# Kernel tuning notes

Measured on AMD Instinct MI355X. Metric: run time of the kernel, lower is better.

The kernel has to match this reference:

```python
import jax, jax.numpy as jnp
import numpy as np

RADIUS = 1.3
N_SAMPLES = 256
STEP = 0.0176


def trilinear(grid, pts):
    """grid: [C, D, H, W]; pts: [M, 3] in [-1, 1] ordered (x, y, z) like torch grid_sample
    (x indexes W, y indexes H, z indexes D), align_corners=True, border padding.
    Returns [M, C]."""
    C, D, H, W = grid.shape
    sizes = jnp.asarray([W, H, D], dtype=pts.dtype)
    co = jnp.clip((pts + 1.0) * 0.5 * (sizes - 1.0), 0.0, sizes - 1.0)
    c0 = jnp.floor(co)
    f = co - c0                                   # [M,3] trilinear weights
    i0 = c0.astype(jnp.int32)
    i1 = jnp.minimum(i0 + 1, jnp.asarray([W - 1, H - 1, D - 1], jnp.int32))
    gf = grid.reshape(C, -1)

    def gat(ix, iy, iz):                          # -> [M, C]
        return gf[:, (iz * H + iy) * W + ix].T

    x0, y0, z0 = i0[:, 0], i0[:, 1], i0[:, 2]
    x1, y1, z1 = i1[:, 0], i1[:, 1], i1[:, 2]
    wx, wy, wz = f[:, 0:1], f[:, 1:2], f[:, 2:3]
    out = (gat(x0, y0, z0) * (1 - wx) * (1 - wy) * (1 - wz)
         + gat(x1, y0, z0) * wx       * (1 - wy) * (1 - wz)
         + gat(x0, y1, z0) * (1 - wx) * wy       * (1 - wz)
         + gat(x1, y1, z0) * wx       * wy       * (1 - wz)
         + gat(x0, y0, z1) * (1 - wx) * (1 - wy) * wz
         + gat(x1, y0, z1) * wx       * (1 - wy) * wz
         + gat(x0, y1, z1) * (1 - wx) * wy       * wz
         + gat(x1, y1, z1) * wx       * wy       * wz)
    return out


def get_intersections(rays_o, dirn):
    """Ray / cube[-R,R]^3 intersection; N_SAMPLES uniform steps from entry point.
    Returns pts [B,N,3], t-values [B,N], validity mask [B,N]."""
    eps = 1e-9
    safe_d = jnp.where(jnp.abs(dirn) < eps, eps, dirn)
    inv = 1.0 / safe_d
    t1 = (-RADIUS - rays_o) * inv
    t2 = (RADIUS - rays_o) * inv
    tmin = jnp.max(jnp.minimum(t1, t2), axis=-1)
    tmax = jnp.min(jnp.maximum(t1, t2), axis=-1)
    tnear = jnp.maximum(tmin, 0.0)
    hit = tmax > tnear                                          # [B]
    t = tnear[:, None] + STEP * jnp.arange(N_SAMPLES, dtype=rays_o.dtype)[None, :]
    pts = rays_o[:, None, :] + t[..., None] * dirn[:, None, :]  # [B,N,3]
    mask = (t < tmax[:, None]) & hit[:, None]
    return pts, t, mask


def setup_inputs() -> dict:
    key = jax.random.key(0)
    ks = jax.random.split(key, 12)
    B, R, GD, FD, NF, HW = 2048, 128, 3, 32, 32, 64
    o = jax.random.normal(ks[0], (B, 3), dtype=jnp.float32)
    rays_o = o / jnp.linalg.norm(o, axis=-1, keepdims=True) * (2.0 * RADIUS)
    rays_d = -rays_o + 0.3 * jax.random.normal(ks[1], (B, 3), dtype=jnp.float32)
    G1 = 0.01 * jax.random.normal(ks[2], (GD, R, R, R), dtype=jnp.float32)
    F = 0.05 * jax.random.normal(ks[3], (FD, NF, NF, NF), dtype=jnp.float32)
    s = 0.1
    return {
        'rays_o': rays_o, 'rays_d': rays_d, 'G1': G1, 'F': F,
        'Wd1': s * jax.random.normal(ks[4], (FD, HW), dtype=jnp.float32),
        'bd1': jnp.zeros((HW,), jnp.float32),
        'Wd2': s * jax.random.normal(ks[5], (HW, 1), dtype=jnp.float32),
        'bd2': jnp.zeros((1,), jnp.float32),
        'Wc1': s * jax.random.normal(ks[6], (FD + 3, HW), dtype=jnp.float32),
        'bc1': jnp.zeros((HW,), jnp.float32),
        'Wc2': s * jax.random.normal(ks[7], (HW, 3), dtype=jnp.float32),
        'bc2': jnp.zeros((3,), jnp.float32),
    }


def reference(rays_o, rays_d, G1, F, Wd1, bd1, Wd2, bd2, Wc1, bc1, Wc2, bc2):
    B = rays_o.shape[0]
    dirn = rays_d / jnp.linalg.norm(rays_d, axis=-1, keepdims=True)
    pts, t, mask = get_intersections(rays_o, dirn)           # [B,N,3],[B,N],[B,N]
    pts_n = (pts / RADIUS).reshape(-1, 3)                     # [M,3] in ~[-1,1]

    # nested multi-grid trilinear lookups: coords -> G1 -> F
    g1v = trilinear(G1, pts_n)                                # [M,3]
    feats = trilinear(F, g1v)                                 # [M,feature_dim]

    # density MLP (1 hidden layer, width 64)
    h = jax.nn.relu(feats @ Wd1 + bd1)
    sigma = (h @ Wd2 + bd2)[:, 0].reshape(B, N_SAMPLES)
    sigma = jnp.where(mask, sigma, 0.0)

    # sigma -> alpha -> compositing weights (abs_light)
    dists = jnp.concatenate([t[:, 1:] - t[:, :-1],
                             jnp.full((B, 1), STEP, t.dtype)], axis=1)
    alpha = 1.0 - jnp.exp(-jax.nn.relu(sigma) * dists)
    T = jnp.cumprod(1.0 - alpha + 1e-10, axis=1)
    T_excl = jnp.concatenate([jnp.ones((B, 1), alpha.dtype), T[:, :-1]], axis=1)
    weights = alpha * T_excl                                  # [B,N]

    # color MLP conditioned on view direction
    dflat = jnp.broadcast_to(dirn[:, None, :], (B, N_SAMPLES, 3)).reshape(-1, 3)
    hc = jax.nn.relu(jnp.concatenate([feats, dflat], axis=-1) @ Wc1 + bc1)
    rgb = jax.nn.sigmoid((hc @ Wc2 + bc2).reshape(B, N_SAMPLES, 3))
    rgb = jnp.where(mask[..., None], rgb, 0.0)

    out = jnp.sum(weights[..., None] * rgb, axis=1)           # [B,3]
    acc = jnp.sum(weights, axis=1)
    return out + (1.0 - acc)[:, None]                         # white background
```

## Files before the change

### kernel.cpp

```cpp
#include <hip/hip_runtime.h>
#include <hip/hip_fp16.h>
#include <math.h>

#define NSAMP 256

typedef _Float16 f16;
typedef _Float16 f16x8 __attribute__((ext_vector_type(8)));
typedef float    f32x4 __attribute__((ext_vector_type(4)));

__global__ __launch_bounds__(256) void transpose_F(
    const float* __restrict__ Fg, float* __restrict__ Ft)
{
    const int j = blockIdx.x * 256 + threadIdx.x;
    float4 o[8];
    #pragma unroll
    for (int q = 0; q < 8; ++q) {
        o[q].x = Fg[(size_t)(4*q+0)*32768 + j];
        o[q].y = Fg[(size_t)(4*q+1)*32768 + j];
        o[q].z = Fg[(size_t)(4*q+2)*32768 + j];
        o[q].w = Fg[(size_t)(4*q+3)*32768 + j];
    }
    float4* dst = (float4*)(Ft + (size_t)j * 32);
    #pragma unroll
    for (int q = 0; q < 8; ++q) dst[q] = o[q];
}

__global__ __launch_bounds__(256) void pack_bfrags(
    const float* __restrict__ Wd1, const float* __restrict__ Wc1,
    f16* __restrict__ Bd, f16* __restrict__ Bc)
{
    const int idx  = threadIdx.x;
    const int nt   = idx >> 6;
    const int lane = idx & 63;
    const int j    = nt*16 + (lane & 15);
    const int k0   = (lane >> 4) * 8;
    f16x8 vd, vc;
    #pragma unroll
    for (int i = 0; i < 8; ++i) {
        vd[i] = (f16)Wd1[(k0+i)*64 + j];
        vc[i] = (f16)Wc1[(k0+i)*64 + j];
    }
    *(f16x8*)(Bd + ((size_t)(nt*64+lane))*8) = vd;
    *(f16x8*)(Bc + ((size_t)(nt*64+lane))*8) = vc;
}

template<bool USE_MFMA>
__global__ __launch_bounds__(256) __attribute__((amdgpu_waves_per_eu(2, 6)))
void nerf_fused(
    const float* __restrict__ rays_o, const float* __restrict__ rays_d,
    const float* __restrict__ G1, const float* __restrict__ Fg,
    const float* __restrict__ Wd1, const float* __restrict__ bd1,
    const float* __restrict__ Wd2, const float* __restrict__ bd2,
    const float* __restrict__ Wc1, const float* __restrict__ bc1,
    const float* __restrict__ Wc2, const float* __restrict__ bc2,
    const float* __restrict__ Ft,
    const f16* __restrict__ Bd, const f16* __restrict__ Bc,
    float* __restrict__ out)
{
    const float RADIUS = 1.3f;
    const float STEP = 0.0176f;

    const int b    = blockIdx.x;
    const int tid  = threadIdx.x;
    const int lane = tid & 63;
    const int wv   = tid >> 6;

    __shared__ __align__(16) f16 feats_lds[256][32];
    __shared__ float sig_lds[256];
    __shared__ f16   rgb_lds[256][4];
    __shared__ float s_wtot[4];
    __shared__ float s_red[4][4];

    const float ox = rays_o[b*3+0], oy = rays_o[b*3+1], oz = rays_o[b*3+2];
    const float rdx = rays_d[b*3+0], rdy = rays_d[b*3+1], rdz = rays_d[b*3+2];
    const float rn  = sqrtf(rdx*rdx + rdy*rdy + rdz*rdz);
    const float dxn = rdx/rn, dyn = rdy/rn, dzn = rdz/rn;

    float sd, inv, t1, t2, tmin, tmax;
    sd = (fabsf(dxn) < 1e-9f) ? 1e-9f : dxn; inv = 1.0f/sd;
    t1 = (-RADIUS - ox)*inv; t2 = (RADIUS - ox)*inv;
    tmin = fminf(t1,t2); tmax = fmaxf(t1,t2);
    sd = (fabsf(dyn) < 1e-9f) ? 1e-9f : dyn; inv = 1.0f/sd;
    t1 = (-RADIUS - oy)*inv; t2 = (RADIUS - oy)*inv;
    tmin = fmaxf(tmin, fminf(t1,t2)); tmax = fminf(tmax, fmaxf(t1,t2));
    sd = (fabsf(dzn) < 1e-9f) ? 1e-9f : dzn; inv = 1.0f/sd;
    t1 = (-RADIUS - oz)*inv; t2 = (RADIUS - oz)*inv;
    tmin = fmaxf(tmin, fminf(t1,t2)); tmax = fminf(tmax, fmaxf(t1,t2));

    const float tnear = fmaxf(tmin, 0.0f);
    const bool  hit   = tmax > tnear;
    const float t     = tnear + STEP * (float)tid;
    const bool  mask  = (t < tmax) && hit;

    const bool wave_active = __any(mask);

    float sigma = 0.0f, rr = 0.0f, rg = 0.0f, rb = 0.0f;

    float feats[32];
    if (wave_active) {
        const float invR = 1.0f / RADIUS;
        const float px = (ox + t*dxn) * invR;
        const float py = (oy + t*dyn) * invR;
        const float pz = (oz + t*dzn) * invR;

        float cox = fminf(fmaxf((px+1.0f)*0.5f*127.0f, 0.0f), 127.0f);
        float coy = fminf(fmaxf((py+1.0f)*0.5f*127.0f, 0.0f), 127.0f);
        float coz = fminf(fmaxf((pz+1.0f)*0.5f*127.0f, 0.0f), 127.0f);
        int x0 = (int)floorf(cox); float fx = cox - (float)x0; int x1 = min(x0+1, 127);
        int y0 = (int)floorf(coy); float fy = coy - (float)y0; int y1 = min(y0+1, 127);
        int z0 = (int)floorf(coz); float fz = coz - (float)z0; int z1 = min(z0+1, 127);

        {
            const float wx0 = 1.0f-fx, wx1 = fx;
            const float wy0 = 1.0f-fy, wy1 = fy;
            const float wz0 = 1.0f-fz, wz1 = fz;
            const float w000 = wx0*wy0*wz0, w100 = wx1*wy0*wz0;
            const float w010 = wx0*wy1*wz0, w110 = wx1*wy1*wz0;
            const float w001 = wx0*wy0*wz1, w101 = wx1*wy0*wz1;
            const float w011 = wx0*wy1*wz1, w111 = wx1*wy1*wz1;
            const int i000 = (z0*128 + y0)*128 + x0;
            const int dxo = x1 - x0;
            const int dyo = (y1 - y0)*128;
            const int dzo = (z1 - z0)*16384;
            const int i100 = i000 + dxo,       i010 = i000 + dyo;
            const int i110 = i000 + dyo + dxo, i001 = i000 + dzo;
            const int i101 = i000 + dzo + dxo, i011 = i000 + dzo + dyo;
            const int i111 = i000 + dzo + dyo + dxo;

            float g[3];
            #pragma unroll
            for (int c = 0; c < 3; ++c) {
                const float* gp = G1 + (size_t)c * 2097152;
                g[c] = w000*gp[i000] + w100*gp[i100] + w010*gp[i010] + w110*gp[i110]
                     + w001*gp[i001] + w101*gp[i101] + w011*gp[i011] + w111*gp[i111];
            }

            cox = fminf(fmaxf((g[0]+1.0f)*0.5f*31.0f, 0.0f), 31.0f);
            coy = fminf(fmaxf((g[1]+1.0f)*0.5f*31.0f, 0.0f), 31.0f);
            coz = fminf(fmaxf((g[2]+1.0f)*0.5f*31.0f, 0.0f), 31.0f);
            x0 = (int)floorf(cox); fx = cox - (float)x0; x1 = min(x0+1, 31);
            y0 = (int)floorf(coy); fy = coy - (float)y0; y1 = min(y0+1, 31);
            z0 = (int)floorf(coz); fz = coz - (float)z0; z1 = min(z0+1, 31);
        }

        #pragma unroll
        for (int c = 0; c < 32; ++c) feats[c] = 0.0f;
        {
            const float wx0 = 1.0f-fx, wx1 = fx;
            const float wy0 = 1.0f-fy, wy1 = fy;
            const float wz0 = 1.0f-fz, wz1 = fz;
            const int j000 = (z0*32 + y0)*32 + x0;
            const int dxo = x1 - x0;
            const int dyo = (y1 - y0)*32;
            const int dzo = (z1 - z0)*1024;

            const int   jidx[8] = { j000,           j000+dxo,
                                    j000+dyo,       j000+dyo+dxo,
                                    j000+dzo,       j000+dzo+dxo,
                                    j000+dzo+dyo,   j000+dzo+dyo+dxo };
            const float jwt[8]  = { wx0*wy0*wz0, wx1*wy0*wz0,
                                    wx0*wy1*wz0, wx1*wy1*wz0,
                                    wx0*wy0*wz1, wx1*wy0*wz1,
                                    wx0*wy1*wz1, wx1*wy1*wz1 };

            if (USE_MFMA) {
                #pragma unroll
                for (int corner = 0; corner < 8; ++corner) {
                    const float4* fp = (const float4*)(Ft + (size_t)jidx[corner] * 32);
                    const float w = jwt[corner];
                    #pragma unroll
                    for (int q = 0; q < 8; ++q) {
                        const float4 v = fp[q];
                        feats[4*q+0] += w * v.x;
                        feats[4*q+1] += w * v.y;
                        feats[4*q+2] += w * v.z;
                        feats[4*q+3] += w * v.w;
                    }
                }
            } else {
                #pragma unroll
                for (int corner = 0; corner < 8; ++corner) {
                    const float w = jwt[corner];
                    const int  j  = jidx[corner];
                    #pragma unroll
                    for (int c = 0; c < 32; ++c)
                        feats[c] += w * Fg[(size_t)c * 32768 + j];
                }
            }
        }
    }

    if (USE_MFMA) {
        if (wave_active) {
            #pragma unroll
            for (int gq = 0; gq < 4; ++gq) {
                f16x8 h;
                #pragma unroll
                for (int i = 0; i < 8; ++i) h[i] = (f16)feats[gq*8+i];
                *(f16x8*)&feats_lds[tid][gq*8] = h;
            }
        }
        __syncthreads();

        if (wave_active) {
            const int lane15 = lane & 15;
            const int laneg  = lane >> 4;

            float bias_d[4], bias_c[4], wd2v[4];
            float wc2r[4], wc2g[4], wc2b[4];
            #pragma unroll
            for (int nt = 0; nt < 4; ++nt) {
                const int j = nt*16 + lane15;
                bias_d[nt] = bd1[j];
                bias_c[nt] = bc1[j] + dxn*Wc1[32*64+j] + dyn*Wc1[33*64+j] + dzn*Wc1[34*64+j];
                wd2v[nt]   = Wd2[j];
                wc2r[nt]   = Wc2[j*3+0];
                wc2g[nt]   = Wc2[j*3+1];
                wc2b[nt]   = Wc2[j*3+2];
            }
            f16x8 bdf[4], bcf[4];
            #pragma unroll
            for (int nt = 0; nt < 4; ++nt) {
                bdf[nt] = *(const f16x8*)(Bd + ((size_t)(nt*64+lane))*8);
                bcf[nt] = *(const f16x8*)(Bc + ((size_t)(nt*64+lane))*8);
            }

            #pragma unroll
            for (int mt = 0; mt < 4; ++mt) {
                const int arow = wv*64 + mt*16 + lane15;
                const f16x8 af = *(const f16x8*)&feats_lds[arow][laneg*8];

                f32x4 accd[4], accc[4];
                #pragma unroll
                for (int nt = 0; nt < 4; ++nt) {
                    const float bdv = bias_d[nt], bcv = bias_c[nt];
                    accd[nt] = (f32x4){bdv, bdv, bdv, bdv};
                    accc[nt] = (f32x4){bcv, bcv, bcv, bcv};
                }
                #pragma unroll
                for (int nt = 0; nt < 4; ++nt) {
                    accd[nt] = __builtin_amdgcn_mfma_f32_16x16x32_f16(af, bdf[nt], accd[nt], 0, 0, 0);
                    accc[nt] = __builtin_amdgcn_mfma_f32_16x16x32_f16(af, bcf[nt], accc[nt], 0, 0, 0);
                }

                float ss[4] = {0.f,0.f,0.f,0.f};
                float sr[4] = {0.f,0.f,0.f,0.f};
                float sg[4] = {0.f,0.f,0.f,0.f};
                float sb[4] = {0.f,0.f,0.f,0.f};
                #pragma unroll
                for (int nt = 0; nt < 4; ++nt) {
                    #pragma unroll
                    for (int reg = 0; reg < 4; ++reg) {
                        const float hd = fmaxf(accd[nt][reg], 0.0f);
                        ss[reg] += hd * wd2v[nt];
                        const float hc = fmaxf(accc[nt][reg], 0.0f);
                        sr[reg] += hc * wc2r[nt];
                        sg[reg] += hc * wc2g[nt];
                        sb[reg] += hc * wc2b[nt];
                    }
                }
                #pragma unroll
                for (int st = 1; st < 16; st <<= 1) {
                    #pragma unroll
                    for (int reg = 0; reg < 4; ++reg) {
                        ss[reg] += __shfl_xor(ss[reg], st, 64);
                        sr[reg] += __shfl_xor(sr[reg], st, 64);
                        sg[reg] += __shfl_xor(sg[reg], st, 64);
                        sb[reg] += __shfl_xor(sb[reg], st, 64);
                    }
                }
                if (lane15 == 0) {
                    const int base = wv*64 + mt*16 + laneg*4;
                    #pragma unroll
                    for (int reg = 0; reg < 4; ++reg) {
                        sig_lds[base+reg]    = ss[reg];
                        rgb_lds[base+reg][0] = (f16)sr[reg];
                        rgb_lds[base+reg][1] = (f16)sg[reg];
                        rgb_lds[base+reg][2] = (f16)sb[reg];
                    }
                }
            }
        }
        __syncthreads();

        {
            const float sv  = sig_lds[tid];
            const float crv = (float)rgb_lds[tid][0] + bc2[0];
            const float cgv = (float)rgb_lds[tid][1] + bc2[1];
            const float cbv = (float)rgb_lds[tid][2] + bc2[2];
            sigma = mask ? (sv + bd2[0]) : 0.0f;
            rr = mask ? 1.0f/(1.0f + expf(-crv)) : 0.0f;
            rg = mask ? 1.0f/(1.0f + expf(-cgv)) : 0.0f;
            rb = mask ? 1.0f/(1.0f + expf(-cbv)) : 0.0f;
        }
    } else {
        if (wave_active) {
            float sg1 = bd2[0], cr = 0.0f, cg = 0.0f, cb = 0.0f;
            for (int j0 = 0; j0 < 64; j0 += 8) {
                float ad[8], ac[8];
                #pragma unroll
                for (int jj = 0; jj < 8; ++jj) {
                    ad[jj] = bd1[j0+jj];
                    ac[jj] = bc1[j0+jj] + dxn*Wc1[32*64 + j0 + jj]
                                        + dyn*Wc1[33*64 + j0 + jj]
                                        + dzn*Wc1[34*64 + j0 + jj];
                }
                #pragma unroll
                for (int k = 0; k < 32; ++k) {
                    const float fv = feats[k];
                    #pragma unroll
                    for (int jj = 0; jj < 8; ++jj) {
                        ad[jj] += fv * Wd1[k*64 + j0 + jj];
                        ac[jj] += fv * Wc1[k*64 + j0 + jj];
                    }
                }
                #pragma unroll
                for (int jj = 0; jj < 8; ++jj) {
                    sg1 += fmaxf(ad[jj], 0.0f) * Wd2[j0+jj];
                    const float hc = fmaxf(ac[jj], 0.0f);
                    cr += hc * Wc2[(j0+jj)*3 + 0];
                    cg += hc * Wc2[(j0+jj)*3 + 1];
                    cb += hc * Wc2[(j0+jj)*3 + 2];
                }
            }
            cr += bc2[0]; cg += bc2[1]; cb += bc2[2];
            sigma = mask ? sg1 : 0.0f;
            rr = mask ? 1.0f/(1.0f + expf(-cr)) : 0.0f;
            rg = mask ? 1.0f/(1.0f + expf(-cg)) : 0.0f;
            rb = mask ? 1.0f/(1.0f + expf(-cb)) : 0.0f;
        }
    }

    const float alpha = 1.0f - expf(-fmaxf(sigma, 0.0f) * STEP);
    float p = 1.0f - alpha + 1e-10f;

    float scan = p;
    #pragma unroll
    for (int off = 1; off < 64; off <<= 1) {
        const float n = __shfl_up(scan, off, 64);
        if (lane >= off) scan *= n;
    }
    if (lane == 63) s_wtot[wv] = scan;
    __syncthreads();

    float pre = 1.0f;
    #pragma unroll
    for (int q = 0; q < 4; ++q) if (q < wv) pre *= s_wtot[q];
    float excl = __shfl_up(scan, 1, 64);
    if (lane == 0) excl = 1.0f;
    const float Texcl = pre * excl;

    const float w = alpha * Texcl;
    float sw  = w;
    float swr = w * rr, swg = w * rg, swb = w * rb;

    #pragma unroll
    for (int off = 32; off > 0; off >>= 1) {
        sw  += __shfl_down(sw,  off, 64);
        swr += __shfl_down(swr, off, 64);
        swg += __shfl_down(swg, off, 64);
        swb += __shfl_down(swb, off, 64);
    }
    if (lane == 0) {
        s_red[wv][0] = sw;  s_red[wv][1] = swr;
        s_red[wv][2] = swg; s_red[wv][3] = swb;
    }
    __syncthreads();
    if (tid == 0) {
        float W = 0.0f, R = 0.0f, Gc = 0.0f, Bc2_ = 0.0f;
        #pragma unroll
        for (int q = 0; q < 4; ++q) {
            W  += s_red[q][0]; R  += s_red[q][1];
            Gc += s_red[q][2]; Bc2_ += s_red[q][3];
        }
        const float bg = 1.0f - W;
        out[b*3+0] = R  + bg;
        out[b*3+1] = Gc + bg;
        out[b*3+2] = Bc2_ + bg;
    }
}

extern "C" void kernel_launch(void* const* d_in, const int* in_sizes, int n_in,
                              void* d_out, int out_size, void* d_ws, size_t ws_size,
                              hipStream_t stream) {
    const float* rays_o = (const float*)d_in[0];
    const float* rays_d = (const float*)d_in[1];
    const float* G1     = (const float*)d_in[2];
    const float* Fg     = (const float*)d_in[3];
    const float* Wd1    = (const float*)d_in[4];
    const float* bd1    = (const float*)d_in[5];
    const float* Wd2    = (const float*)d_in[6];
    const float* bd2    = (const float*)d_in[7];
    const float* Wc1    = (const float*)d_in[8];
    const float* bc1    = (const float*)d_in[9];
    const float* Wc2    = (const float*)d_in[10];
    const float* bc2    = (const float*)d_in[11];
    float* out = (float*)d_out;

    const int B = in_sizes[0] / 3;
    const size_t ft_bytes = (size_t)32768 * 32 * sizeof(float);
    const size_t bf_bytes = (size_t)4 * 64 * 8 * sizeof(f16);

    if (ws_size >= ft_bytes + 2*bf_bytes) {
        float* Ft = (float*)d_ws;
        f16*   Bd = (f16*)((char*)d_ws + ft_bytes);
        f16*   Bc = (f16*)((char*)d_ws + ft_bytes + bf_bytes);
        transpose_F<<<dim3(128), dim3(256), 0, stream>>>(Fg, Ft);
        pack_bfrags<<<dim3(1), dim3(256), 0, stream>>>(Wd1, Wc1, Bd, Bc);
        nerf_fused<true><<<dim3(B), dim3(NSAMP), 0, stream>>>(
            rays_o, rays_d, G1, Fg, Wd1, bd1, Wd2, bd2, Wc1, bc1, Wc2, bc2,
            Ft, Bd, Bc, out);
    } else {
        nerf_fused<false><<<dim3(B), dim3(NSAMP), 0, stream>>>(
            rays_o, rays_d, G1, Fg, Wd1, bd1, Wd2, bd2, Wc1, bc1, Wc2, bc2,
            Fg, (const f16*)d_ws, (const f16*)d_ws, out);
    }
}
```

Before: 144.9 us.

## Split fused NeRF kernel into gather+MLP and compositing passes with fp16 interleaved coarse grid

Adds a pre-pass that converts the coarse 3-channel grid G1 into an interleaved fp16x4 layout, so each trilinear corner becomes a single 8-byte load. The fused kernel is split in two. A gather kernel runs the grid lookups and MFMA MLPs, with each wave taking samples from a different ray and whole-wave early exit for missed rays. A second kernel does sigmoid, transmittance scan and compositing. This aims to cut gather traffic and improve load balance and latency hiding. The cost is an extra transpose pass over the 8M-element grid each call, a round-trip of per-sample results through global memory, fp16 rounding of coarse grid values, and a larger workspace requirement.

```diff
diff --git a/kernel.cpp b/kernel.cpp
--- a/kernel.cpp
+++ b/kernel.cpp
@@ -5,6 +5,7 @@
 #define NSAMP 256
 
 typedef _Float16 f16;
+typedef _Float16 f16x4 __attribute__((ext_vector_type(4)));
 typedef _Float16 f16x8 __attribute__((ext_vector_type(8)));
 typedef float    f32x4 __attribute__((ext_vector_type(4)));
 
@@ -23,6 +24,18 @@
     float4* dst = (float4*)(Ft + (size_t)j * 32);
     #pragma unroll
     for (int q = 0; q < 8; ++q) dst[q] = o[q];
+}
+
+__global__ __launch_bounds__(256) void transpose_G1h(
+    const float* __restrict__ G1, f16x4* __restrict__ G1t)
+{
+    const int v = blockIdx.x * 256 + threadIdx.x;
+    f16x4 o;
+    o[0] = (f16)G1[v];
+    o[1] = (f16)G1[2097152 + v];
+    o[2] = (f16)G1[2*2097152 + v];
+    o[3] = (f16)0.0f;
+    G1t[v] = o;
 }
 
 __global__ __launch_bounds__(256) void pack_bfrags(
@@ -42,6 +55,305 @@
     }
     *(f16x8*)(Bd + ((size_t)(nt*64+lane))*8) = vd;
     *(f16x8*)(Bc + ((size_t)(nt*64+lane))*8) = vc;
+}
+
+__global__ __launch_bounds__(256) __attribute__((amdgpu_waves_per_eu(2, 6)))
+void nerf_gather(
+    const float* __restrict__ rays_o, const float* __restrict__ rays_d,
+    const f16x4* __restrict__ G1t, const float* __restrict__ Ft,
+    const float* __restrict__ bd1, const float* __restrict__ Wd2,
+    const float* __restrict__ bd2,
+    const float* __restrict__ Wc1, const float* __restrict__ bc1,
+    const float* __restrict__ Wc2,
+    const f16* __restrict__ Bd, const f16* __restrict__ Bc,
+    float4* __restrict__ samp)
+{
+    const float RADIUS = 1.3f;
+    const float STEP = 0.0176f;
+
+    const int tid  = threadIdx.x;
+    const int lane = tid & 63;
+    const int wv   = tid >> 6;
+
+    int ray = blockIdx.x + wv * (gridDim.x >> 2);
+    if (ray >= (int)gridDim.x) ray -= gridDim.x;
+
+    __shared__ __align__(16) f16 feats_lds[256][40];
+
+    const float ox = rays_o[ray*3+0], oy = rays_o[ray*3+1], oz = rays_o[ray*3+2];
+    const float rdx = rays_d[ray*3+0], rdy = rays_d[ray*3+1], rdz = rays_d[ray*3+2];
+    const float rn  = sqrtf(rdx*rdx + rdy*rdy + rdz*rdz);
+    const float dxn = rdx/rn, dyn = rdy/rn, dzn = rdz/rn;
+
+    float sd, inv, t1, t2, tmin, tmax;
+    sd = (fabsf(dxn) < 1e-9f) ? 1e-9f : dxn; inv = 1.0f/sd;
+    t1 = (-RADIUS - ox)*inv; t2 = (RADIUS - ox)*inv;
+    tmin = fminf(t1,t2); tmax = fmaxf(t1,t2);
+    sd = (fabsf(dyn) < 1e-9f) ? 1e-9f : dyn; inv = 1.0f/sd;
+    t1 = (-RADIUS - oy)*inv; t2 = (RADIUS - oy)*inv;
+    tmin = fmaxf(tmin, fminf(t1,t2)); tmax = fminf(tmax, fmaxf(t1,t2));
+    sd = (fabsf(dzn) < 1e-9f) ? 1e-9f : dzn; inv = 1.0f/sd;
+    t1 = (-RADIUS - oz)*inv; t2 = (RADIUS - oz)*inv;
+    tmin = fmaxf(tmin, fminf(t1,t2)); tmax = fminf(tmax, fmaxf(t1,t2));
+
+    const float tnear = fmaxf(tmin, 0.0f);
+    const bool  hit   = tmax > tnear;
+    const float t     = tnear + STEP * (float)tid;
+    const bool  mask  = (t < tmax) && hit;
+
+    if (!__any(mask)) {
+        samp[(size_t)ray*NSAMP + tid] = (float4){0.f, 0.f, 0.f, 0.f};
+        return;
+    }
+
+    float feats[32];
+    {
+        const float invR = 1.0f / RADIUS;
+        const float px = (ox + t*dxn) * invR;
+        const float py = (oy + t*dyn) * invR;
+        const float pz = (oz + t*dzn) * invR;
+
+        float cox = fminf(fmaxf((px+1.0f)*0.5f*127.0f, 0.0f), 127.0f);
+        float coy = fminf(fmaxf((py+1.0f)*0.5f*127.0f, 0.0f), 127.0f);
+        float coz = fminf(fmaxf((pz+1.0f)*0.5f*127.0f, 0.0f), 127.0f);
+        int x0 = (int)floorf(cox); float fx = cox - (float)x0; int x1 = min(x0+1, 127);
+        int y0 = (int)floorf(coy); float fy = coy - (float)y0; int y1 = min(y0+1, 127);
+        int z0 = (int)floorf(coz); float fz = coz - (float)z0; int z1 = min(z0+1, 127);
+
+        {
+            const float wx0 = 1.0f-fx, wx1 = fx;
+            const float wy0 = 1.0f-fy, wy1 = fy;
+            const float wz0 = 1.0f-fz, wz1 = fz;
+            const float w000 = wx0*wy0*wz0, w100 = wx1*wy0*wz0;
+            const float w010 = wx0*wy1*wz0, w110 = wx1*wy1*wz0;
+            const float w001 = wx0*wy0*wz1, w101 = wx1*wy0*wz1;
+            const float w011 = wx0*wy1*wz1, w111 = wx1*wy1*wz1;
+            const int i000 = (z0*128 + y0)*128 + x0;
+            const int dxo = x1 - x0;
+            const int dyo = (y1 - y0)*128;
+            const int dzo = (z1 - z0)*16384;
+
+            const f16x4 v000 = G1t[i000];
+            const f16x4 v100 = G1t[i000 + dxo];
+            const f16x4 v010 = G1t[i000 + dyo];
+            const f16x4 v110 = G1t[i000 + dyo + dxo];
+            const f16x4 v001 = G1t[i000 + dzo];
+            const f16x4 v101 = G1t[i000 + dzo + dxo];
+            const f16x4 v011 = G1t[i000 + dzo + dyo];
+            const f16x4 v111 = G1t[i000 + dzo + dyo + dxo];
+
+            float g[3];
+            #pragma unroll
+            for (int c = 0; c < 3; ++c) {
+                g[c] = w000*(float)v000[c] + w100*(float)v100[c]
+                     + w010*(float)v010[c] + w110*(float)v110[c]
+                     + w001*(float)v001[c] + w101*(float)v101[c]
+                     + w011*(float)v011[c] + w111*(float)v111[c];
+            }
+
+            cox = fminf(fmaxf((g[0]+1.0f)*0.5f*31.0f, 0.0f), 31.0f);
+            coy = fminf(fmaxf((g[1]+1.0f)*0.5f*31.0f, 0.0f), 31.0f);
+            coz = fminf(fmaxf((g[2]+1.0f)*0.5f*31.0f, 0.0f), 31.0f);
+            x0 = (int)floorf(cox); fx = cox - (float)x0; x1 = min(x0+1, 31);
+            y0 = (int)floorf(coy); fy = coy - (float)y0; y1 = min(y0+1, 31);
+            z0 = (int)floorf(coz); fz = coz - (float)z0; z1 = min(z0+1, 31);
+        }
+
+        #pragma unroll
+        for (int c = 0; c < 32; ++c) feats[c] = 0.0f;
+        {
+            const float wx0 = 1.0f-fx, wx1 = fx;
+            const float wy0 = 1.0f-fy, wy1 = fy;
+            const float wz0 = 1.0f-fz, wz1 = fz;
+            const int j000 = (z0*32 + y0)*32 + x0;
+            const int dxo = x1 - x0;
+            const int dyo = (y1 - y0)*32;
+            const int dzo = (z1 - z0)*1024;
+
+            const int   jidx[8] = { j000,           j000+dxo,
+                                    j000+dyo,       j000+dyo+dxo,
+                                    j000+dzo,       j000+dzo+dxo,
+                                    j000+dzo+dyo,   j000+dzo+dyo+dxo };
+            const float jwt[8]  = { wx0*wy0*wz0, wx1*wy0*wz0,
+                                    wx0*wy1*wz0, wx1*wy1*wz0,
+                                    wx0*wy0*wz1, wx1*wy0*wz1,
+                                    wx0*wy1*wz1, wx1*wy1*wz1 };
+
+            #pragma unroll
+            for (int corner = 0; corner < 8; ++corner) {
+                const float4* fp = (const float4*)(Ft + (size_t)jidx[corner] * 32);
+                const float w = jwt[corner];
+                #pragma unroll
+                for (int q = 0; q < 8; ++q) {
+                    const float4 v = fp[q];
+                    feats[4*q+0] += w * v.x;
+                    feats[4*q+1] += w * v.y;
+                    feats[4*q+2] += w * v.z;
+                    feats[4*q+3] += w * v.w;
+                }
+            }
+        }
+    }
+
+    #pragma unroll
+    for (int gq = 0; gq < 4; ++gq) {
+        f16x8 h;
+        #pragma unroll
+        for (int i = 0; i < 8; ++i) h[i] = (f16)feats[gq*8+i];
+        *(f16x8*)&feats_lds[tid][gq*8] = h;
+    }
+
+    {
+        const int lane15 = lane & 15;
+        const int laneg  = lane >> 4;
+
+        float bias_d[4], bias_c[4], wd2v[4];
+        float wc2r[4], wc2g[4], wc2b[4];
+        #pragma unroll
+        for (int nt = 0; nt < 4; ++nt) {
+            const int j = nt*16 + lane15;
+            bias_d[nt] = bd1[j];
+            bias_c[nt] = bc1[j] + dxn*Wc1[32*64+j] + dyn*Wc1[33*64+j] + dzn*Wc1[34*64+j];
+            wd2v[nt]   = Wd2[j];
+            wc2r[nt]   = Wc2[j*3+0];
+            wc2g[nt]   = Wc2[j*3+1];
+            wc2b[nt]   = Wc2[j*3+2];
+        }
+        f16x8 bdf[4], bcf[4];
+        #pragma unroll
+        for (int nt = 0; nt < 4; ++nt) {
+            bdf[nt] = *(const f16x8*)(Bd + ((size_t)(nt*64+lane))*8);
+            bcf[nt] = *(const f16x8*)(Bc + ((size_t)(nt*64+lane))*8);
+        }
+        const float bd2v = bd2[0];
+
+        #pragma unroll
+        for (int mt = 0; mt < 4; ++mt) {
+            const int arow = wv*64 + mt*16 + lane15;
+            const f16x8 af = *(const f16x8*)&feats_lds[arow][laneg*8];
+
+            f32x4 accd[4], accc[4];
+            #pragma unroll
+            for (int nt = 0; nt < 4; ++nt) {
+                const float bdv = bias_d[nt], bcv = bias_c[nt];
+                accd[nt] = (f32x4){bdv, bdv, bdv, bdv};
+                accc[nt] = (f32x4){bcv, bcv, bcv, bcv};
+            }
+            #pragma unroll
+            for (int nt = 0; nt < 4; ++nt) {
+                accd[nt] = __builtin_amdgcn_mfma_f32_16x16x32_f16(af, bdf[nt], accd[nt], 0, 0, 0);
+                accc[nt] = __builtin_amdgcn_mfma_f32_16x16x32_f16(af, bcf[nt], accc[nt], 0, 0, 0);
+            }
+
+            float ss[4] = {0.f,0.f,0.f,0.f};
+            float sr[4] = {0.f,0.f,0.f,0.f};
+            float sg[4] = {0.f,0.f,0.f,0.f};
+            float sb[4] = {0.f,0.f,0.f,0.f};
+            #pragma unroll
+            for (int nt = 0; nt < 4; ++nt) {
+                #pragma unroll
+                for (int reg = 0; reg < 4; ++reg) {
+                    const float hd = fmaxf(accd[nt][reg], 0.0f);
+                    ss[reg] += hd * wd2v[nt];
+                    const float hc = fmaxf(accc[nt][reg], 0.0f);
+                    sr[reg] += hc * wc2r[nt];
+                    sg[reg] += hc * wc2g[nt];
+                    sb[reg] += hc * wc2b[nt];
+                }
+            }
+            #pragma unroll
+            for (int st = 1; st < 16; st <<= 1) {
+                #pragma unroll
+                for (int reg = 0; reg < 4; ++reg) {
+                    ss[reg] += __shfl_xor(ss[reg], st, 64);
+                    sr[reg] += __shfl_xor(sr[reg], st, 64);
+                    sg[reg] += __shfl_xor(sg[reg], st, 64);
+                    sb[reg] += __shfl_xor(sb[reg], st, 64);
+                }
+            }
+            if (lane15 == 0) {
+                const int base = wv*64 + mt*16 + laneg*4;
+                #pragma unroll
+                for (int reg = 0; reg < 4; ++reg) {
+                    const int   row = base + reg;
+                    const float tr  = tnear + STEP * (float)row;
+                    const bool  mr  = (tr < tmax) && hit;
+                    float4 o;
+                    o.x = mr ? (ss[reg] + bd2v) : 0.0f;
+                    o.y = sr[reg]; o.z = sg[reg]; o.w = sb[reg];
+                    samp[(size_t)ray*NSAMP + row] = o;
+                }
+            }
+        }
+    }
+}
+
+__global__ __launch_bounds__(256) void nerf_comp(
+    const float4* __restrict__ samp, const float* __restrict__ bc2,
+    float* __restrict__ out)
+{
+    const float STEP = 0.0176f;
+    const int b    = blockIdx.x;
+    const int tid  = threadIdx.x;
+    const int lane = tid & 63;
+    const int wv   = tid >> 6;
+
+    __shared__ float s_wtot[4];
+    __shared__ float s_red[4][4];
+
+    const float4 v = samp[(size_t)b*NSAMP + tid];
+    const float sigma = v.x;
+    const float rr = 1.0f/(1.0f + expf(-(v.y + bc2[0])));
+    const float rg = 1.0f/(1.0f + expf(-(v.z + bc2[1])));
+    const float rb = 1.0f/(1.0f + expf(-(v.w + bc2[2])));
+
+    const float alpha = 1.0f - expf(-fmaxf(sigma, 0.0f) * STEP);
+    float p = 1.0f - alpha + 1e-10f;
+
+    float scan = p;
+    #pragma unroll
+    for (int off = 1; off < 64; off <<= 1) {
+        const float n = __shfl_up(scan, off, 64);
+        if (lane >= off) scan *= n;
+    }
+    if (lane == 63) s_wtot[wv] = scan;
+    __syncthreads();
+
+    float pre = 1.0f;
+    #pragma unroll
+    for (int q = 0; q < 4; ++q) if (q < wv) pre *= s_wtot[q];
+    float excl = __shfl_up(scan, 1, 64);
+    if (lane == 0) excl = 1.0f;
+    const float Texcl = pre * excl;
+
+    const float w = alpha * Texcl;
+    float sw  = w;
+    float swr = w * rr, swg = w * rg, swb = w * rb;
+
+    #pragma unroll
+    for (int off = 32; off > 0; off >>= 1) {
+        sw  += __shfl_down(sw,  off, 64);
+        swr += __shfl_down(swr, off, 64);
+        swg += __shfl_down(swg, off, 64);
+        swb += __shfl_down(swb, off, 64);
+    }
+    if (lane == 0) {
+        s_red[wv][0] = sw;  s_red[wv][1] = swr;
+        s_red[wv][2] = swg; s_red[wv][3] = swb;
+    }
+    __syncthreads();
+    if (tid == 0) {
+        float W = 0.0f, R = 0.0f, Gc = 0.0f, Bc_ = 0.0f;
+        #pragma unroll
+        for (int q = 0; q < 4; ++q) {
+            W  += s_red[q][0]; R  += s_red[q][1];
+            Gc += s_red[q][2]; Bc_ += s_red[q][3];
+        }
+        const float bg = 1.0f - W;
+        out[b*3+0] = R   + bg;
+        out[b*3+1] = Gc  + bg;
+        out[b*3+2] = Bc_ + bg;
+    }
 }
 
 template<bool USE_MFMA>
@@ -65,7 +377,7 @@
     const int lane = tid & 63;
     const int wv   = tid >> 6;
 
-    __shared__ __align__(16) f16 feats_lds[256][32];
+    __shared__ __align__(16) f16 feats_lds[256][40];
     __shared__ float sig_lds[256];
     __shared__ f16   rgb_lds[256][4];
     __shared__ float s_wtot[4];
@@ -398,10 +710,24 @@
     float* out = (float*)d_out;
 
     const int B = in_sizes[0] / 3;
-    const size_t ft_bytes = (size_t)32768 * 32 * sizeof(float);
-    const size_t bf_bytes = (size_t)4 * 64 * 8 * sizeof(f16);
-
-    if (ws_size >= ft_bytes + 2*bf_bytes) {
+    const size_t ft_bytes   = (size_t)32768 * 32 * sizeof(float);
+    const size_t bf_bytes   = (size_t)4 * 64 * 8 * sizeof(f16);
+    const size_t g1th_bytes = (size_t)2097152 * sizeof(f16x4);
+    const size_t samp_bytes = (size_t)B * NSAMP * sizeof(float4);
+
+    if (ws_size >= ft_bytes + 2*bf_bytes + g1th_bytes + samp_bytes) {
+        float*  Ft   = (float*)d_ws;
+        f16*    Bd   = (f16*)((char*)d_ws + ft_bytes);
+        f16*    Bc   = (f16*)((char*)d_ws + ft_bytes + bf_bytes);
+        f16x4*  G1t  = (f16x4*)((char*)d_ws + ft_bytes + 2*bf_bytes);
+        float4* samp = (float4*)((char*)d_ws + ft_bytes + 2*bf_bytes + g1th_bytes);
+        transpose_F<<<dim3(128), dim3(256), 0, stream>>>(Fg, Ft);
+        transpose_G1h<<<dim3(8192), dim3(256), 0, stream>>>(G1, G1t);
+        pack_bfrags<<<dim3(1), dim3(256), 0, stream>>>(Wd1, Wc1, Bd, Bc);
+        nerf_gather<<<dim3(B), dim3(NSAMP), 0, stream>>>(
+            rays_o, rays_d, G1t, Ft, bd1, Wd2, bd2, Wc1, bc1, Wc2, Bd, Bc, samp);
+        nerf_comp<<<dim3(B), dim3(NSAMP), 0, stream>>>(samp, bc2, out);
+    } else if (ws_size >= ft_bytes + 2*bf_bytes) {
         float* Ft = (float*)d_ws;
         f16*   Bd = (f16*)((char*)d_ws + ft_bytes);
         f16*   Bc = (f16*)((char*)d_ws + ft_bytes + bf_bytes);
```

New measurement: 150.4 us. 1.04x slower.
